# Kernel tuning notes

Hardware: AMD Instinct MI355X
Metric: run time of the kernel (lower is better)

Reference implementation:

```python
import jax, jax.numpy as jnp
import numpy as np

B, T, C = 4, 2048, 1024
E, H, K = 8, 2048, 2


def setup_inputs() -> dict:
    key = jax.random.key(0)
    ks = jax.random.split(key, 7)
    s_in = 1.0 / np.sqrt(C)
    s_hid = 1.0 / np.sqrt(H)
    return {
        "x": jax.random.normal(ks[0], (B, T, C), dtype=jnp.float32),
        "gate_w": jax.random.uniform(ks[1], (C, E), jnp.float32, -s_in, s_in),
        "gate_b": jnp.zeros((E,), jnp.float32),
        "w1": jax.random.uniform(ks[2], (E, C, H), jnp.float32, -s_in, s_in),
        "b1": jax.random.uniform(ks[3], (E, H), jnp.float32, -s_in, s_in),
        "w2": jax.random.uniform(ks[4], (E, H, C), jnp.float32, -s_hid, s_hid),
        "b2": jax.random.uniform(ks[5], (E, C), jnp.float32, -s_hid, s_hid),
    }


def reference(x, gate_w, gate_b, w1, b1, w2, b2):
    b, t, c = x.shape
    xf = x.reshape(b * t, c)  # (N, C)

    # TopKGate: softmax over expert logits, take top-k gate values/indices
    logits = xf @ gate_w + gate_b              # (N, E)
    probs = jax.nn.softmax(logits, axis=-1)
    gates, expert_idx = jax.lax.top_k(probs, K)  # (N, K) each

    # Dense all-experts MLP (faithful to the original which runs every expert)
    h = jax.nn.relu(jnp.einsum('nc,ech->neh', xf, w1) + b1)  # (N, E, H)
    expert_out = jnp.einsum('neh,ehc->nec', h, w2) + b2      # (N, E, C)

    # Combine weights: scatter top-k gate values into (N, E), then weighted sum
    onehot = jax.nn.one_hot(expert_idx, E, dtype=xf.dtype)   # (N, K, E)
    weights = jnp.einsum('nk,nke->ne', gates, onehot)        # (N, E)
    out = jnp.einsum('ne,nec->nc', weights, expert_out)      # (N, C)
    return out.reshape(b, t, c)
```

## Files before the change

### kernel.cpp

```cpp
#include <hip/hip_runtime.h>
#include <cstdint>
#include <cstddef>

typedef __attribute__((ext_vector_type(8))) short short8;
typedef __attribute__((ext_vector_type(4))) float f32x4;
typedef __attribute__((ext_vector_type(4))) float flt4;

#define DEV __device__ __forceinline__

constexpr int C_ = 1024, E_ = 8, H_ = 2048, K_TOP = 2;
constexpr int N_ = 8192;
constexpr int NK_ = N_ * K_TOP;
constexpr int HB_ = 32;

DEV unsigned short f2bf(float f){
  unsigned u = __float_as_uint(f);
  u += 0x7fffu + ((u >> 16) & 1u);
  return (unsigned short)(u >> 16);
}

DEV void gload16(const void* g, void* l){
  __builtin_amdgcn_global_load_lds((const __attribute__((address_space(1))) unsigned int*)g,
                                   (__attribute__((address_space(3))) unsigned int*)l,
                                   16, 0, 0);
}

__global__ void cvt_x_kernel(const float* __restrict__ s, unsigned short* __restrict__ d){
  size_t i = ((size_t)blockIdx.x * blockDim.x + threadIdx.x) * 8;
  flt4 v0 = *(const flt4*)(s + i);
  flt4 v1 = *(const flt4*)(s + i + 4);
  short8 o;
  o[0]=f2bf(v0[0]); o[1]=f2bf(v0[1]); o[2]=f2bf(v0[2]); o[3]=f2bf(v0[3]);
  o[4]=f2bf(v1[0]); o[5]=f2bf(v1[1]); o[6]=f2bf(v1[2]); o[7]=f2bf(v1[3]);
  *(short8*)(d + i) = o;
}

__global__ void tconv_kernel(const float* __restrict__ src, unsigned short* __restrict__ dst,
                             int R, int S){
  __shared__ float tile[32][33];
  int e = blockIdx.z;
  int r0 = blockIdx.y * 32, s0 = blockIdx.x * 32;
  const float* se = src + (size_t)e * R * S;
  unsigned short* de = dst + (size_t)e * R * S;
  int tx = threadIdx.x & 31, ty = threadIdx.x >> 5;
  #pragma unroll
  for (int i = 0; i < 4; i++){
    int r = ty + i * 8;
    tile[r][tx] = se[(size_t)(r0 + r) * S + s0 + tx];
  }
  __syncthreads();
  #pragma unroll
  for (int i = 0; i < 4; i++){
    int s = ty + i * 8;
    de[(size_t)(s0 + s) * R + r0 + tx] = f2bf(tile[tx][s]);
  }
}

__global__ void gate_kernel(const float* __restrict__ x, const float* __restrict__ gw,
                            const float* __restrict__ gb,
                            int* __restrict__ tok_e, float* __restrict__ tok_g){
  int lane = threadIdx.x & 63;
  int n = blockIdx.x * 4 + (threadIdx.x >> 6);
  const float* xr = x + (size_t)n * C_;
  float acc[E_];
  #pragma unroll
  for (int e = 0; e < E_; e++) acc[e] = 0.f;
  #pragma unroll 4
  for (int j = 0; j < C_ / 64; j++){
    int c = lane + j * 64;
    float xv = xr[c];
    flt4 g0 = *(const flt4*)(gw + (size_t)c * E_);
    flt4 g1 = *(const flt4*)(gw + (size_t)c * E_ + 4);
    acc[0] += xv * g0[0]; acc[1] += xv * g0[1]; acc[2] += xv * g0[2]; acc[3] += xv * g0[3];
    acc[4] += xv * g1[0]; acc[5] += xv * g1[1]; acc[6] += xv * g1[2]; acc[7] += xv * g1[3];
  }
  #pragma unroll
  for (int e = 0; e < E_; e++)
    #pragma unroll
    for (int off = 32; off > 0; off >>= 1)
      acc[e] += __shfl_xor(acc[e], off, 64);
  if (lane == 0){
    float l[E_], p[E_];
    float m = -1e30f;
    #pragma unroll
    for (int e = 0; e < E_; e++){ l[e] = acc[e] + gb[e]; m = fmaxf(m, l[e]); }
    float s = 0.f;
    #pragma unroll
    for (int e = 0; e < E_; e++){ p[e] = expf(l[e] - m); s += p[e]; }
    float inv = 1.f / s;
    int e0 = 0; float m0 = p[0];
    #pragma unroll
    for (int e = 1; e < E_; e++) if (p[e] > m0){ m0 = p[e]; e0 = e; }
    int e1 = -1; float m1 = -1.f;
    #pragma unroll
    for (int e = 0; e < E_; e++) if (e != e0 && p[e] > m1){ m1 = p[e]; e1 = e; }
    tok_e[2*n]   = e0; tok_g[2*n]   = m0 * inv;
    tok_e[2*n+1] = e1; tok_g[2*n+1] = m1 * inv;
  }
}

__global__ void hist_kernel(const int* __restrict__ tok_e, int* __restrict__ blockhist){
  __shared__ int h[E_];
  if (threadIdx.x < E_) h[threadIdx.x] = 0;
  __syncthreads();
  int n = blockIdx.x * 256 + threadIdx.x;
  int e0 = tok_e[2*n], e1 = tok_e[2*n+1];
  atomicAdd(&h[e0], 1);
  atomicAdd(&h[e1], 1);
  __syncthreads();
  if (threadIdx.x < E_) blockhist[blockIdx.x * E_ + threadIdx.x] = h[threadIdx.x];
}

__global__ void scan2_kernel(const int* __restrict__ blockhist, int* __restrict__ counts,
                             int* __restrict__ offsets, int* __restrict__ blockbase){
  if (threadIdx.x == 0){
    int tot[E_];
    for (int e = 0; e < E_; e++){
      int s = 0;
      for (int b = 0; b < HB_; b++) s += blockhist[b * E_ + e];
      tot[e] = s;
    }
    int s = 0;
    for (int e = 0; e < E_; e++){ counts[e] = tot[e]; offsets[e] = s; s += tot[e]; }
    for (int e = 0; e < E_; e++){
      int cur = offsets[e];
      for (int b = 0; b < HB_; b++){ blockbase[b * E_ + e] = cur; cur += blockhist[b * E_ + e]; }
    }
  }
}

__global__ void build_kernel(const int* __restrict__ tok_e, const float* __restrict__ tok_g,
                             const int* __restrict__ blockbase,
                             int* __restrict__ list_tok, float* __restrict__ list_gate){
  __shared__ int cur[E_];
  if (threadIdx.x < E_) cur[threadIdx.x] = blockbase[blockIdx.x * E_ + threadIdx.x];
  __syncthreads();
  int n = blockIdx.x * 256 + threadIdx.x;
  #pragma unroll
  for (int k = 0; k < K_TOP; k++){
    int e = tok_e[2*n + k];
    int pos = atomicAdd(&cur[e], 1);
    list_tok[pos] = n;
    list_gate[pos] = tok_g[2*n + k];
  }
}

template<bool FIRST>
__global__ __launch_bounds__(256, 2)
void moe_gemm(const unsigned short* __restrict__ Abase,
              const unsigned short* __restrict__ Bbase,
              const float* __restrict__ bias,
              const int* __restrict__ counts, const int* __restrict__ offsets,
              const int* __restrict__ list_tok, const float* __restrict__ list_gate,
              unsigned short* __restrict__ hbuf, float* __restrict__ out){
  constexpr int K  = FIRST ? C_ : H_;
  constexpr int ND = FIRST ? H_ : C_;
  __shared__ unsigned char smem[32768];
  int e = blockIdx.z;
  int ne = counts[e];
  int row0 = blockIdx.y * 128;
  if (row0 >= ne) return;
  int off = offsets[e];
  int col0 = blockIdx.x * 128;
  int tid = threadIdx.x;
  int lane = tid & 63, wave = tid >> 6;
  int wm = wave >> 1, wn = wave & 1;
  int lr = lane & 15, lk = lane >> 4;

  int rr = tid >> 3;
  int chunk = (tid & 7) ^ (rr & 7);
  const unsigned short* Bexp = Bbase + (size_t)e * ND * K;
  const unsigned short* agsrc[4];
  const unsigned short* bgsrc[4];
  #pragma unroll
  for (int j = 0; j < 4; j++){
    int r = j * 32 + rr;
    int rc = min(row0 + r, ne - 1);
    size_t arow = FIRST ? (size_t)list_tok[off + rc] * C_ : (size_t)(off + rc) * H_;
    agsrc[j] = Abase + arow + chunk * 8;
    bgsrc[j] = Bexp + (size_t)(col0 + r) * K + chunk * 8;
  }
  unsigned char* Adst = smem + wave * 1024;
  unsigned char* Bdst = smem + 16384 + wave * 1024;

  f32x4 acc[4][4];
  #pragma unroll
  for (int a = 0; a < 4; a++)
    #pragma unroll
    for (int b = 0; b < 4; b++) acc[a][b] = (f32x4){0.f,0.f,0.f,0.f};

  for (int k0 = 0; k0 < K; k0 += 64){
    __syncthreads();
    #pragma unroll
    for (int j = 0; j < 4; j++) gload16(agsrc[j] + k0, Adst + j * 4096);
    #pragma unroll
    for (int j = 0; j < 4; j++) gload16(bgsrc[j] + k0, Bdst + j * 4096);
    __syncthreads();
    #pragma unroll
    for (int s = 0; s < 2; s++){
      short8 av[4], bv[4];
      int kx = ((s * 4 + lk) ^ (lr & 7)) * 16;
      #pragma unroll
      for (int fm = 0; fm < 4; fm++){
        int row = wm * 64 + fm * 16 + lr;
        av[fm] = *(const short8*)(smem + row * 128 + kx);
      }
      #pragma unroll
      for (int fn = 0; fn < 4; fn++){
        int col = wn * 64 + fn * 16 + lr;
        bv[fn] = *(const short8*)(smem + 16384 + col * 128 + kx);
      }
      #pragma unroll
      for (int fm = 0; fm < 4; fm++)
        #pragma unroll
        for (int fn = 0; fn < 4; fn++)
          acc[fm][fn] = __builtin_amdgcn_mfma_f32_16x16x32_bf16(av[fm], bv[fn], acc[fm][fn], 0, 0, 0);
    }
  }

  if (FIRST){
    #pragma unroll
    for (int fm = 0; fm < 4; fm++){
      int rbase = row0 + wm*64 + fm*16 + lk*4;
      #pragma unroll
      for (int fn = 0; fn < 4; fn++){
        int colb = col0 + wn*64 + fn*16 + lr;
        float bv2 = bias[e*ND + colb];
        #pragma unroll
        for (int i = 0; i < 4; i++){
          int r = rbase + i;
          if (r < ne){
            float v = acc[fm][fn][i] + bv2;
            v = v > 0.f ? v : 0.f;
            hbuf[(size_t)(off + r)*H_ + colb] = f2bf(v);
          }
        }
      }
    }
  } else {
    #pragma unroll
    for (int fm = 0; fm < 4; fm++){
      int rbase = row0 + wm*64 + fm*16 + lk*4;
      #pragma unroll
      for (int i = 0; i < 4; i++){
        int r = rbase + i;
        if (r < ne){
          int pos = off + r;
          int tok = list_tok[pos];
          float g = list_gate[pos];
          float* orow = out + (size_t)tok * C_;
          #pragma unroll
          for (int fn = 0; fn < 4; fn++){
            int colb = col0 + wn*64 + fn*16 + lr;
            float v = (acc[fm][fn][i] + bias[e*ND + colb]) * g;
            atomicAdd(orow + colb, v);
          }
        }
      }
    }
  }
}

extern "C" void kernel_launch(void* const* d_in, const int* in_sizes, int n_in,
                              void* d_out, int out_size, void* d_ws, size_t ws_size,
                              hipStream_t stream){
  const float* x  = (const float*)d_in[0];
  const float* gw = (const float*)d_in[1];
  const float* gb = (const float*)d_in[2];
  const float* w1 = (const float*)d_in[3];
  const float* b1 = (const float*)d_in[4];
  const float* w2 = (const float*)d_in[5];
  const float* b2 = (const float*)d_in[6];
  float* out = (float*)d_out;

  char* p = (char*)d_ws;
  unsigned short* xb   = (unsigned short*)p; p += (size_t)N_*C_*2;
  unsigned short* w1t  = (unsigned short*)p; p += (size_t)E_*C_*H_*2;
  unsigned short* w2t  = (unsigned short*)p; p += (size_t)E_*C_*H_*2;
  unsigned short* hbuf = (unsigned short*)p; p += (size_t)NK_*H_*2;
  int*   tok_e     = (int*)p;   p += (size_t)NK_*4;
  float* tok_g     = (float*)p; p += (size_t)NK_*4;
  int*   list_tok  = (int*)p;   p += (size_t)NK_*4;
  float* list_gate = (float*)p; p += (size_t)NK_*4;
  int*   counts    = (int*)p;   p += 256;
  int*   offsets   = (int*)p;   p += 256;
  int*   blockhist = (int*)p;   p += HB_*E_*4;
  int*   blockbase = (int*)p;   p += HB_*E_*4;

  hipMemsetAsync(out, 0, (size_t)out_size * sizeof(float), stream);

  cvt_x_kernel<<<(N_*C_/8)/256, 256, 0, stream>>>(x, xb);
  tconv_kernel<<<dim3(H_/32, C_/32, E_), 256, 0, stream>>>(w1, w1t, C_, H_);
  tconv_kernel<<<dim3(C_/32, H_/32, E_), 256, 0, stream>>>(w2, w2t, H_, C_);
  gate_kernel<<<N_/4, 256, 0, stream>>>(x, gw, gb, tok_e, tok_g);
  hist_kernel<<<HB_, 256, 0, stream>>>(tok_e, blockhist);
  scan2_kernel<<<1, 64, 0, stream>>>(blockhist, counts, offsets, blockbase);
  build_kernel<<<HB_, 256, 0, stream>>>(tok_e, tok_g, blockbase, list_tok, list_gate);

  moe_gemm<true ><<<dim3(H_/128, N_/128, E_), 256, 0, stream>>>(xb,   w1t, b1, counts, offsets, list_tok, list_gate, hbuf, out);
  moe_gemm<false><<<dim3(C_/128, N_/128, E_), 256, 0, stream>>>(hbuf, w2t, b2, counts, offsets, list_tok, list_gate, hbuf, out);
}
```

Before: 357.4 us.

## Enlarge MoE GEMM tiles to 256x256 with double-buffered LDS prefetch

The grouped expert GEMMs move from 128x128 tiles with 256 threads to 256x256 tiles with 512 threads (8 waves, each computing 128x64). LDS is double-buffered across 128 KB so the next K-slice is fetched with global_load_lds while the current one feeds the MFMAs, and one barrier per iteration replaces two. Larger tiles raise data reuse per load, but 128 KB of LDS allows only one block per CU. Per-expert row padding to 256 also wastes more work, and the grid has fewer blocks to balance.

```diff
diff --git a/kernel.cpp b/kernel.cpp
--- a/kernel.cpp
+++ b/kernel.cpp
@@ -146,7 +146,7 @@
 }
 
 template<bool FIRST>
-__global__ __launch_bounds__(256, 2)
+__global__ __launch_bounds__(512, 2)
 void moe_gemm(const unsigned short* __restrict__ Abase,
               const unsigned short* __restrict__ Bbase,
               const float* __restrict__ bias,
@@ -155,82 +155,91 @@
               unsigned short* __restrict__ hbuf, float* __restrict__ out){
   constexpr int K  = FIRST ? C_ : H_;
   constexpr int ND = FIRST ? H_ : C_;
-  __shared__ unsigned char smem[32768];
+  constexpr int NT = K / 64;
+  __shared__ unsigned char smem[131072];
   int e = blockIdx.z;
   int ne = counts[e];
-  int row0 = blockIdx.y * 128;
+  int row0 = blockIdx.y * 256;
   if (row0 >= ne) return;
   int off = offsets[e];
-  int col0 = blockIdx.x * 128;
+  int col0 = blockIdx.x * 256;
   int tid = threadIdx.x;
   int lane = tid & 63, wave = tid >> 6;
-  int wm = wave >> 1, wn = wave & 1;
+  int wm = wave >> 2, wn = wave & 3;
   int lr = lane & 15, lk = lane >> 4;
 
-  int rr = tid >> 3;
-  int chunk = (tid & 7) ^ (rr & 7);
+  int chunk = (tid & 7) ^ ((tid >> 3) & 7);
   const unsigned short* Bexp = Bbase + (size_t)e * ND * K;
   const unsigned short* agsrc[4];
   const unsigned short* bgsrc[4];
   #pragma unroll
   for (int j = 0; j < 4; j++){
-    int r = j * 32 + rr;
+    int r = j * 64 + (tid >> 3);
     int rc = min(row0 + r, ne - 1);
     size_t arow = FIRST ? (size_t)list_tok[off + rc] * C_ : (size_t)(off + rc) * H_;
     agsrc[j] = Abase + arow + chunk * 8;
     bgsrc[j] = Bexp + (size_t)(col0 + r) * K + chunk * 8;
   }
-  unsigned char* Adst = smem + wave * 1024;
-  unsigned char* Bdst = smem + 16384 + wave * 1024;
-
-  f32x4 acc[4][4];
-  #pragma unroll
-  for (int a = 0; a < 4; a++)
+  unsigned char* Ad = smem + wave * 1024;
+  unsigned char* Bd = smem + 32768 + wave * 1024;
+
+  f32x4 acc[8][4];
+  #pragma unroll
+  for (int a = 0; a < 8; a++)
     #pragma unroll
     for (int b = 0; b < 4; b++) acc[a][b] = (f32x4){0.f,0.f,0.f,0.f};
 
-  for (int k0 = 0; k0 < K; k0 += 64){
+  #pragma unroll
+  for (int j = 0; j < 4; j++) gload16(agsrc[j], Ad + j * 8192);
+  #pragma unroll
+  for (int j = 0; j < 4; j++) gload16(bgsrc[j], Bd + j * 8192);
+  __syncthreads();
+
+  int cur = 0;
+  for (int t = 0; t < NT; ++t){
+    if (t + 1 < NT){
+      int nb = (cur ^ 1) * 65536;
+      int kn = (t + 1) * 64;
+      #pragma unroll
+      for (int j = 0; j < 4; j++) gload16(agsrc[j] + kn, Ad + nb + j * 8192);
+      #pragma unroll
+      for (int j = 0; j < 4; j++) gload16(bgsrc[j] + kn, Bd + nb + j * 8192);
+    }
+    const unsigned char* Ab = smem + cur * 65536;
+    const unsigned char* Bb = Ab + 32768;
+    #pragma unroll
+    for (int s = 0; s < 2; s++){
+      short8 av[8], bv[4];
+      int kx = ((s * 4 + lk) ^ (lr & 7)) * 16;
+      #pragma unroll
+      for (int m = 0; m < 8; m++)
+        av[m] = *(const short8*)(Ab + (wm * 128 + m * 16 + lr) * 128 + kx);
+      #pragma unroll
+      for (int n = 0; n < 4; n++)
+        bv[n] = *(const short8*)(Bb + (wn * 64 + n * 16 + lr) * 128 + kx);
+      #pragma unroll
+      for (int m = 0; m < 8; m++)
+        #pragma unroll
+        for (int n = 0; n < 4; n++)
+          acc[m][n] = __builtin_amdgcn_mfma_f32_16x16x32_bf16(av[m], bv[n], acc[m][n], 0, 0, 0);
+    }
     __syncthreads();
-    #pragma unroll
-    for (int j = 0; j < 4; j++) gload16(agsrc[j] + k0, Adst + j * 4096);
-    #pragma unroll
-    for (int j = 0; j < 4; j++) gload16(bgsrc[j] + k0, Bdst + j * 4096);
-    __syncthreads();
-    #pragma unroll
-    for (int s = 0; s < 2; s++){
-      short8 av[4], bv[4];
-      int kx = ((s * 4 + lk) ^ (lr & 7)) * 16;
-      #pragma unroll
-      for (int fm = 0; fm < 4; fm++){
-        int row = wm * 64 + fm * 16 + lr;
-        av[fm] = *(const short8*)(smem + row * 128 + kx);
-      }
-      #pragma unroll
-      for (int fn = 0; fn < 4; fn++){
-        int col = wn * 64 + fn * 16 + lr;
-        bv[fn] = *(const short8*)(smem + 16384 + col * 128 + kx);
-      }
-      #pragma unroll
-      for (int fm = 0; fm < 4; fm++)
-        #pragma unroll
-        for (int fn = 0; fn < 4; fn++)
-          acc[fm][fn] = __builtin_amdgcn_mfma_f32_16x16x32_bf16(av[fm], bv[fn], acc[fm][fn], 0, 0, 0);
-    }
+    cur ^= 1;
   }
 
   if (FIRST){
     #pragma unroll
-    for (int fm = 0; fm < 4; fm++){
-      int rbase = row0 + wm*64 + fm*16 + lk*4;
-      #pragma unroll
-      for (int fn = 0; fn < 4; fn++){
-        int colb = col0 + wn*64 + fn*16 + lr;
+    for (int m = 0; m < 8; m++){
+      int rbase = row0 + wm*128 + m*16 + lk*4;
+      #pragma unroll
+      for (int n = 0; n < 4; n++){
+        int colb = col0 + wn*64 + n*16 + lr;
         float bv2 = bias[e*ND + colb];
         #pragma unroll
         for (int i = 0; i < 4; i++){
           int r = rbase + i;
           if (r < ne){
-            float v = acc[fm][fn][i] + bv2;
+            float v = acc[m][n][i] + bv2;
             v = v > 0.f ? v : 0.f;
             hbuf[(size_t)(off + r)*H_ + colb] = f2bf(v);
           }
@@ -239,8 +248,8 @@
     }
   } else {
     #pragma unroll
-    for (int fm = 0; fm < 4; fm++){
-      int rbase = row0 + wm*64 + fm*16 + lk*4;
+    for (int m = 0; m < 8; m++){
+      int rbase = row0 + wm*128 + m*16 + lk*4;
       #pragma unroll
       for (int i = 0; i < 4; i++){
         int r = rbase + i;
@@ -250,9 +259,9 @@
           float g = list_gate[pos];
           float* orow = out + (size_t)tok * C_;
           #pragma unroll
-          for (int fn = 0; fn < 4; fn++){
-            int colb = col0 + wn*64 + fn*16 + lr;
-            float v = (acc[fm][fn][i] + bias[e*ND + colb]) * g;
+          for (int n = 0; n < 4; n++){
+            int colb = col0 + wn*64 + n*16 + lr;
+            float v = (acc[m][n][i] + bias[e*ND + colb]) * g;
             atomicAdd(orow + colb, v);
           }
         }
@@ -297,6 +306,6 @@
   scan2_kernel<<<1, 64, 0, stream>>>(blockhist, counts, offsets, blockbase);
   build_kernel<<<HB_, 256, 0, stream>>>(tok_e, tok_g, blockbase, list_tok, list_gate);
 
-  moe_gemm<true ><<<dim3(H_/128, N_/128, E_), 256, 0, stream>>>(xb,   w1t, b1, counts, offsets, list_tok, list_gate, hbuf, out);
-  moe_gemm<false><<<dim3(C_/128, N_/128, E_), 256, 0, stream>>>(hbuf, w2t, b2, counts, offsets, list_tok, list_gate, hbuf, out);
-}
+  moe_gemm<true ><<<dim3(H_/256, N_/256, E_), 512, 0, stream>>>(xb,   w1t, b1, counts, offsets, list_tok, list_gate, hbuf, out);
+  moe_gemm<false><<<dim3(C_/256, N_/256, E_), 512, 0, stream>>>(hbuf, w2t, b2, counts, offsets, list_tok, list_gate, hbuf, out);
+}
```

New measurement: 414.6 us. +16.0%, slower.

## Use persistent grid-stride MoE GEMM blocks over active tiles per expert

Applied to the files above, without the earlier changes.

Replaces the dense 3D grid, where most blocks exit early because their row tile exceeds the expert's token count, with a fixed 1024-block launch. Each block is pinned to one expert and walks that expert's active tiles with a stride of 128. Launch bounds also rise from 2 to 4 blocks per SM, which can reduce register availability. Load balance now depends on the per-expert token counts, since each expert gets an equal share of blocks regardless of its workload.

```diff
diff --git a/kernel.cpp b/kernel.cpp
--- a/kernel.cpp
+++ b/kernel.cpp
@@ -146,114 +146,121 @@
 }
 
 template<bool FIRST>
-__global__ __launch_bounds__(256, 2)
+__global__ __launch_bounds__(256, 4)
 void moe_gemm(const unsigned short* __restrict__ Abase,
               const unsigned short* __restrict__ Bbase,
               const float* __restrict__ bias,
               const int* __restrict__ counts, const int* __restrict__ offsets,
               const int* __restrict__ list_tok, const float* __restrict__ list_gate,
               unsigned short* __restrict__ hbuf, float* __restrict__ out){
-  constexpr int K  = FIRST ? C_ : H_;
-  constexpr int ND = FIRST ? H_ : C_;
+  constexpr int K   = FIRST ? C_ : H_;
+  constexpr int ND  = FIRST ? H_ : C_;
+  constexpr int TX  = ND / 128;
+  constexpr int LTX = FIRST ? 4 : 3;
   __shared__ unsigned char smem[32768];
-  int e = blockIdx.z;
+
+  int b = blockIdx.x;
+  int e    = b & 7;
+  int slot = b >> 3;
   int ne = counts[e];
-  int row0 = blockIdx.y * 128;
-  if (row0 >= ne) return;
   int off = offsets[e];
-  int col0 = blockIdx.x * 128;
+  int nty  = (ne + 127) >> 7;
+  int nact = nty << LTX;
+  const unsigned short* Bexp = Bbase + (size_t)e * ND * K;
+
   int tid = threadIdx.x;
   int lane = tid & 63, wave = tid >> 6;
   int wm = wave >> 1, wn = wave & 1;
   int lr = lane & 15, lk = lane >> 4;
-
   int rr = tid >> 3;
   int chunk = (tid & 7) ^ (rr & 7);
-  const unsigned short* Bexp = Bbase + (size_t)e * ND * K;
-  const unsigned short* agsrc[4];
-  const unsigned short* bgsrc[4];
-  #pragma unroll
-  for (int j = 0; j < 4; j++){
-    int r = j * 32 + rr;
-    int rc = min(row0 + r, ne - 1);
-    size_t arow = FIRST ? (size_t)list_tok[off + rc] * C_ : (size_t)(off + rc) * H_;
-    agsrc[j] = Abase + arow + chunk * 8;
-    bgsrc[j] = Bexp + (size_t)(col0 + r) * K + chunk * 8;
-  }
-  unsigned char* Adst = smem + wave * 1024;
-  unsigned char* Bdst = smem + 16384 + wave * 1024;
-
-  f32x4 acc[4][4];
-  #pragma unroll
-  for (int a = 0; a < 4; a++)
-    #pragma unroll
-    for (int b = 0; b < 4; b++) acc[a][b] = (f32x4){0.f,0.f,0.f,0.f};
-
-  for (int k0 = 0; k0 < K; k0 += 64){
-    __syncthreads();
-    #pragma unroll
-    for (int j = 0; j < 4; j++) gload16(agsrc[j] + k0, Adst + j * 4096);
-    #pragma unroll
-    for (int j = 0; j < 4; j++) gload16(bgsrc[j] + k0, Bdst + j * 4096);
-    __syncthreads();
-    #pragma unroll
-    for (int s = 0; s < 2; s++){
-      short8 av[4], bv[4];
-      int kx = ((s * 4 + lk) ^ (lr & 7)) * 16;
+
+  for (int w = slot; w < nact; w += 128){
+    int bx = w & (TX - 1);
+    int by = w >> LTX;
+    int row0 = by * 128, col0 = bx * 128;
+
+    const unsigned short* agsrc[4];
+    const unsigned short* bgsrc[4];
+    #pragma unroll
+    for (int j = 0; j < 4; j++){
+      int r = j * 32 + rr;
+      int rc = min(row0 + r, ne - 1);
+      size_t arow = FIRST ? (size_t)list_tok[off + rc] * C_ : (size_t)(off + rc) * H_;
+      agsrc[j] = Abase + arow + chunk * 8;
+      bgsrc[j] = Bexp + (size_t)(col0 + r) * K + chunk * 8;
+    }
+    unsigned char* Adst = smem + wave * 1024;
+    unsigned char* Bdst = smem + 16384 + wave * 1024;
+
+    f32x4 acc[4][4];
+    #pragma unroll
+    for (int a = 0; a < 4; a++)
+      #pragma unroll
+      for (int c2 = 0; c2 < 4; c2++) acc[a][c2] = (f32x4){0.f,0.f,0.f,0.f};
+
+    for (int k0 = 0; k0 < K; k0 += 64){
+      __syncthreads();
+      #pragma unroll
+      for (int j = 0; j < 4; j++) gload16(agsrc[j] + k0, Adst + j * 4096);
+      #pragma unroll
+      for (int j = 0; j < 4; j++) gload16(bgsrc[j] + k0, Bdst + j * 4096);
+      __syncthreads();
+      #pragma unroll
+      for (int s = 0; s < 2; s++){
+        short8 av[4], bv[4];
+        int kx = ((s * 4 + lk) ^ (lr & 7)) * 16;
+        #pragma unroll
+        for (int fm = 0; fm < 4; fm++)
+          av[fm] = *(const short8*)(smem + (wm * 64 + fm * 16 + lr) * 128 + kx);
+        #pragma unroll
+        for (int fn = 0; fn < 4; fn++)
+          bv[fn] = *(const short8*)(smem + 16384 + (wn * 64 + fn * 16 + lr) * 128 + kx);
+        #pragma unroll
+        for (int fm = 0; fm < 4; fm++)
+          #pragma unroll
+          for (int fn = 0; fn < 4; fn++)
+            acc[fm][fn] = __builtin_amdgcn_mfma_f32_16x16x32_bf16(av[fm], bv[fn], acc[fm][fn], 0, 0, 0);
+      }
+    }
+
+    if (FIRST){
       #pragma unroll
       for (int fm = 0; fm < 4; fm++){
-        int row = wm * 64 + fm * 16 + lr;
-        av[fm] = *(const short8*)(smem + row * 128 + kx);
+        int rbase = row0 + wm*64 + fm*16 + lk*4;
+        #pragma unroll
+        for (int fn = 0; fn < 4; fn++){
+          int colb = col0 + wn*64 + fn*16 + lr;
+          float bv2 = bias[e*ND + colb];
+          #pragma unroll
+          for (int i = 0; i < 4; i++){
+            int r = rbase + i;
+            if (r < ne){
+              float v = acc[fm][fn][i] + bv2;
+              v = v > 0.f ? v : 0.f;
+              hbuf[(size_t)(off + r)*H_ + colb] = f2bf(v);
+            }
+          }
+        }
       }
-      #pragma unroll
-      for (int fn = 0; fn < 4; fn++){
-        int col = wn * 64 + fn * 16 + lr;
-        bv[fn] = *(const short8*)(smem + 16384 + col * 128 + kx);
-      }
-      #pragma unroll
-      for (int fm = 0; fm < 4; fm++)
-        #pragma unroll
-        for (int fn = 0; fn < 4; fn++)
-          acc[fm][fn] = __builtin_amdgcn_mfma_f32_16x16x32_bf16(av[fm], bv[fn], acc[fm][fn], 0, 0, 0);
-    }
-  }
-
-  if (FIRST){
-    #pragma unroll
-    for (int fm = 0; fm < 4; fm++){
-      int rbase = row0 + wm*64 + fm*16 + lk*4;
-      #pragma unroll
-      for (int fn = 0; fn < 4; fn++){
-        int colb = col0 + wn*64 + fn*16 + lr;
-        float bv2 = bias[e*ND + colb];
+    } else {
+      #pragma unroll
+      for (int fm = 0; fm < 4; fm++){
+        int rbase = row0 + wm*64 + fm*16 + lk*4;
         #pragma unroll
         for (int i = 0; i < 4; i++){
           int r = rbase + i;
           if (r < ne){
-            float v = acc[fm][fn][i] + bv2;
-            v = v > 0.f ? v : 0.f;
-            hbuf[(size_t)(off + r)*H_ + colb] = f2bf(v);
-          }
-        }
-      }
-    }
-  } else {
-    #pragma unroll
-    for (int fm = 0; fm < 4; fm++){
-      int rbase = row0 + wm*64 + fm*16 + lk*4;
-      #pragma unroll
-      for (int i = 0; i < 4; i++){
-        int r = rbase + i;
-        if (r < ne){
-          int pos = off + r;
-          int tok = list_tok[pos];
-          float g = list_gate[pos];
-          float* orow = out + (size_t)tok * C_;
-          #pragma unroll
-          for (int fn = 0; fn < 4; fn++){
-            int colb = col0 + wn*64 + fn*16 + lr;
-            float v = (acc[fm][fn][i] + bias[e*ND + colb]) * g;
-            atomicAdd(orow + colb, v);
+            int pos = off + r;
+            int tok = list_tok[pos];
+            float g = list_gate[pos];
+            float* orow = out + (size_t)tok * C_;
+            #pragma unroll
+            for (int fn = 0; fn < 4; fn++){
+              int colb = col0 + wn*64 + fn*16 + lr;
+              float v = (acc[fm][fn][i] + bias[e*ND + colb]) * g;
+              atomicAdd(orow + colb, v);
+            }
           }
         }
       }
@@ -297,6 +304,6 @@
   scan2_kernel<<<1, 64, 0, stream>>>(blockhist, counts, offsets, blockbase);
   build_kernel<<<HB_, 256, 0, stream>>>(tok_e, tok_g, blockbase, list_tok, list_gate);
 
-  moe_gemm<true ><<<dim3(H_/128, N_/128, E_), 256, 0, stream>>>(xb,   w1t, b1, counts, offsets, list_tok, list_gate, hbuf, out);
-  moe_gemm<false><<<dim3(C_/128, N_/128, E_), 256, 0, stream>>>(hbuf, w2t, b2, counts, offsets, list_tok, list_gate, hbuf, out);
-}
+  moe_gemm<true ><<<1024, 256, 0, stream>>>(xb,   w1t, b1, counts, offsets, list_tok, list_gate, hbuf, out);
+  moe_gemm<false><<<1024, 256, 0, stream>>>(hbuf, w2t, b2, counts, offsets, list_tok, list_gate, hbuf, out);
+}
```

Result: slower. 465.1 us (+30.1%).

## Double-buffer LDS tiles in MoE GEMM and remap blocks by XCD

Applied to the files above, without the earlier changes.

The MoE grouped GEMM now uses two 32KB LDS buffers, so the next K-tile's global-to-LDS loads are issued before computing on the current tile, with one barrier per iteration instead of two. Block indices are also remapped so that blocks consecutive in the remapped order are spaced eight launch positions apart, which on MI355X's round-robin XCD dispatch groups related tiles on the same XCD for L2 reuse. Doubling shared memory to 64KB may reduce occupancy below the two blocks per CU requested by launch bounds.

```diff
diff --git a/kernel.cpp b/kernel.cpp
--- a/kernel.cpp
+++ b/kernel.cpp
@@ -153,22 +153,32 @@
               const int* __restrict__ counts, const int* __restrict__ offsets,
               const int* __restrict__ list_tok, const float* __restrict__ list_gate,
               unsigned short* __restrict__ hbuf, float* __restrict__ out){
-  constexpr int K  = FIRST ? C_ : H_;
-  constexpr int ND = FIRST ? H_ : C_;
-  __shared__ unsigned char smem[32768];
-  int e = blockIdx.z;
+  constexpr int K   = FIRST ? C_ : H_;
+  constexpr int ND  = FIRST ? H_ : C_;
+  constexpr int NT  = K / 64;
+  constexpr int GX  = ND / 128;
+  constexpr int LGX = FIRST ? 4 : 3;
+  constexpr int GY  = N_ / 128;
+  __shared__ unsigned char smem[65536];
+
+  int lin  = blockIdx.x + GX * (blockIdx.y + GY * blockIdx.z);
+  int work = (lin & 7) * (GX * GY) + (lin >> 3);
+  int bx = work & (GX - 1);
+  int by = (work >> LGX) & (GY - 1);
+  int e  = work >> (LGX + 6);
+
   int ne = counts[e];
-  int row0 = blockIdx.y * 128;
+  int row0 = by * 128;
   if (row0 >= ne) return;
   int off = offsets[e];
-  int col0 = blockIdx.x * 128;
+  int col0 = bx * 128;
   int tid = threadIdx.x;
   int lane = tid & 63, wave = tid >> 6;
   int wm = wave >> 1, wn = wave & 1;
   int lr = lane & 15, lk = lane >> 4;
-
   int rr = tid >> 3;
   int chunk = (tid & 7) ^ (rr & 7);
+
   const unsigned short* Bexp = Bbase + (size_t)e * ND * K;
   const unsigned short* agsrc[4];
   const unsigned short* bgsrc[4];
@@ -180,42 +190,50 @@
     agsrc[j] = Abase + arow + chunk * 8;
     bgsrc[j] = Bexp + (size_t)(col0 + r) * K + chunk * 8;
   }
-  unsigned char* Adst = smem + wave * 1024;
-  unsigned char* Bdst = smem + 16384 + wave * 1024;
 
   f32x4 acc[4][4];
   #pragma unroll
   for (int a = 0; a < 4; a++)
     #pragma unroll
-    for (int b = 0; b < 4; b++) acc[a][b] = (f32x4){0.f,0.f,0.f,0.f};
-
-  for (int k0 = 0; k0 < K; k0 += 64){
-    __syncthreads();
-    #pragma unroll
-    for (int j = 0; j < 4; j++) gload16(agsrc[j] + k0, Adst + j * 4096);
-    #pragma unroll
-    for (int j = 0; j < 4; j++) gload16(bgsrc[j] + k0, Bdst + j * 4096);
-    __syncthreads();
+    for (int c2 = 0; c2 < 4; c2++) acc[a][c2] = (f32x4){0.f,0.f,0.f,0.f};
+
+  {
+    unsigned char* Ad = smem + wave * 1024;
+    #pragma unroll
+    for (int j = 0; j < 4; j++) gload16(agsrc[j], Ad + j * 4096);
+    #pragma unroll
+    for (int j = 0; j < 4; j++) gload16(bgsrc[j], Ad + 16384 + j * 4096);
+  }
+  __syncthreads();
+
+  for (int t = 0; t < NT; ++t){
+    if (t + 1 < NT){
+      unsigned char* Ad = smem + ((t + 1) & 1) * 32768 + wave * 1024;
+      int kn = (t + 1) * 64;
+      #pragma unroll
+      for (int j = 0; j < 4; j++) gload16(agsrc[j] + kn, Ad + j * 4096);
+      #pragma unroll
+      for (int j = 0; j < 4; j++) gload16(bgsrc[j] + kn, Ad + 16384 + j * 4096);
+    }
+    const unsigned char* Ab = smem + (t & 1) * 32768;
+    const unsigned char* Bb = Ab + 16384;
     #pragma unroll
     for (int s = 0; s < 2; s++){
       short8 av[4], bv[4];
       int kx = ((s * 4 + lk) ^ (lr & 7)) * 16;
       #pragma unroll
-      for (int fm = 0; fm < 4; fm++){
-        int row = wm * 64 + fm * 16 + lr;
-        av[fm] = *(const short8*)(smem + row * 128 + kx);
-      }
-      #pragma unroll
-      for (int fn = 0; fn < 4; fn++){
-        int col = wn * 64 + fn * 16 + lr;
-        bv[fn] = *(const short8*)(smem + 16384 + col * 128 + kx);
-      }
+      for (int fm = 0; fm < 4; fm++)
+        av[fm] = *(const short8*)(Ab + (wm * 64 + fm * 16 + lr) * 128 + kx);
+      #pragma unroll
+      for (int fn = 0; fn < 4; fn++)
+        bv[fn] = *(const short8*)(Bb + (wn * 64 + fn * 16 + lr) * 128 + kx);
       #pragma unroll
       for (int fm = 0; fm < 4; fm++)
         #pragma unroll
         for (int fn = 0; fn < 4; fn++)
           acc[fm][fn] = __builtin_amdgcn_mfma_f32_16x16x32_bf16(av[fm], bv[fn], acc[fm][fn], 0, 0, 0);
     }
+    __syncthreads();
   }
 
   if (FIRST){
```

Result: slower. 367.7 us (+2.9%).
